# Kernel tuning notes

Measured on AMD Instinct MI355X. Metric: run time of the kernel, lower is better.

## Reference

```python
import jax, jax.numpy as jnp
import numpy as np

# ---- PGA G(3,0,1) tables (metric: e0^2=0, e1^2=e2^2=e3^2=1) ----
METRIC = np.array([0.0, 1.0, 1.0, 1.0])
BLADES = [(), (0,), (1,), (2,), (3,), (0, 1), (0, 2), (0, 3), (1, 2), (1, 3),
          (2, 3), (0, 1, 2), (0, 1, 3), (0, 2, 3), (1, 2, 3), (0, 1, 2, 3)]
IDX = {b: i for i, b in enumerate(BLADES)}


def _sort_sign(lst):
    lst = list(lst)
    sign = 1
    for i in range(len(lst)):
        for j in range(len(lst) - 1 - i):
            if lst[j] > lst[j + 1]:
                lst[j], lst[j + 1] = lst[j + 1], lst[j]
                sign = -sign
    return lst, sign


def _gp(a, b):
    lst, sign = _sort_sign(list(a) + list(b))
    coef = float(sign)
    out, i = [], 0
    while i < len(lst):
        if i + 1 < len(lst) and lst[i] == lst[i + 1]:
            coef *= METRIC[lst[i]]
            i += 2
        else:
            out.append(lst[i])
            i += 1
    return tuple(out), coef


def _outer(a, b):
    if set(a) & set(b):
        return (), 0.0
    lst, sign = _sort_sign(list(a) + list(b))
    return tuple(lst), float(sign)


def _build_tables():
    G = np.zeros((16, 16, 16))
    O = np.zeros((16, 16, 16))
    for i, a in enumerate(BLADES):
        for j, b in enumerate(BLADES):
            bl, c = _gp(a, b)
            if c != 0.0:
                G[IDX[bl], i, j] = c
            bl, c = _outer(a, b)
            if c != 0.0:
                O[IDX[bl], i, j] = c
    # right complement dual: a ^ dual(a) = e0123
    D = np.zeros((16, 16))
    for i, a in enumerate(BLADES):
        comp = tuple(sorted(set(range(4)) - set(a)))
        _, s = _outer(a, comp)
        D[IDX[comp], i] = s
    Dinv = np.linalg.inv(D)
    # join(x, y) = undual(dual(x) ^ dual(y))
    J = np.einsum('km,mpq,pi,qj->kij', Dinv, O, D, D)
    # 9 Pin(3,0,1)-equivariant linear basis maps:
    # 5 grade projections + 4 maps (e0 wedge grade-k part without e0)
    B = np.zeros((9, 16, 16))
    grades = [len(b) for b in BLADES]
    for w in range(5):
        for i, g in enumerate(grades):
            if g == w:
                B[w, i, i] = 1.0
    for w in range(4):
        for i, a in enumerate(BLADES):
            if len(a) == w and 0 not in a:
                bl, c = _outer((0,), a)
                B[5 + w, IDX[bl], i] = c
    return jnp.asarray(G), jnp.asarray(J), jnp.asarray(B)


GP_TBL, JOIN_TBL, EQUI_BASIS = _build_tables()


def equi_linear(x, W):
    # x: [..., c, 16], W: [o, c, 9] -> [..., o, 16]
    M = jnp.einsum('ocw,wab->oacb', W, EQUI_BASIS)  # small: [o,16,c,16]
    return jnp.einsum('oacb,...cb->...oa', M, x)


def setup_inputs() -> dict:
    key = jax.random.key(0)
    k1, k2, k3, k4 = jax.random.split(key, 4)
    B, S, C = 8, 8192, 32
    x = jax.random.normal(k1, (B, S, C, 16), dtype=jnp.float32)
    ref_mv = jax.random.normal(k2, (B, S, 1, 16), dtype=jnp.float32)
    W_bil = jax.random.normal(k3, (2 * 32, C, 9), dtype=jnp.float32) / np.sqrt(9 * C)
    W_out = jax.random.normal(k4, (C, 32, 9), dtype=jnp.float32) / np.sqrt(9 * 32)
    return {"x": x, "ref_mv": ref_mv, "W_bil": W_bil, "W_out": W_out}


def reference(x, ref_mv, W_bil, W_out):
    # project hidden channels -> 2*intermediate = 64 channels
    h = equi_linear(x, W_bil)                      # [B,S,64,16]
    lg, rg, lj, rj = jnp.split(h, 4, axis=-2)      # each [B,S,16,16]
    gp = jnp.einsum('kij,...ci,...cj->...ck', GP_TBL, lg, rg)
    jn = ref_mv[..., 14:15] * jnp.einsum('kij,...ci,...cj->...ck', JOIN_TBL, lj, rj)
    y = jnp.concatenate([gp, jn], axis=-2)         # [B,S,32,16]
    return equi_linear(y, W_out)                   # [B,S,32,16]
```

## Files before the change

### kernel.cpp

```cpp
#include <hip/hip_runtime.h>

typedef float v2f __attribute__((ext_vector_type(2)));

namespace pga {
constexpr int MASKA[16] = {0,1,2,4,8,3,5,9,6,10,12,7,11,13,14,15};
constexpr int IMASK[16] = {0,1,2,5,3,6,8,11,4,7,9,12,10,13,14,15};
constexpr int GR[16]    = {0,1,1,1,1,2,2,2,2,2,2,3,3,3,3,4};

constexpr int osign(int a, int b){
  int c = 0;
  for (int j = 0; j < 4; ++j) if ((b>>j)&1)
    for (int i = j+1; i < 4; ++i) if ((a>>i)&1) ++c;
  return (c&1) ? -1 : 1;
}

struct Tab {
  float gpc[16][16]; int gpk[16][16];
  float jnc[16][16]; int jnk[16][16];
};

constexpr Tab build(){
  Tab t{};
  for (int i = 0; i < 16; ++i) for (int j = 0; j < 16; ++j) {
    const int ma = MASKA[i], mb = MASKA[j];
    if (ma & mb & 1) { t.gpc[i][j] = 0.0f; t.gpk[i][j] = 0; }
    else { t.gpk[i][j] = IMASK[ma^mb]; t.gpc[i][j] = (float)osign(ma, mb); }
    const int ua = 15^ma, ub = 15^mb;
    if (ua & ub) { t.jnc[i][j] = 0.0f; t.jnk[i][j] = 0; }
    else {
      const int sa = osign(ma, ua), sb = osign(mb, ub);
      const int m  = ua | ub;
      const int tt = osign(ua, ub);
      const int r  = 15^m;
      const int sr = osign(r, m);
      t.jnk[i][j] = IMASK[r];
      t.jnc[i][j] = (float)(sa*sb*tt*sr);
    }
  }
  return t;
}
constexpr Tab TAB = build();
constexpr int PS[8] = {0,2,3,4,8,9,10,14};
constexpr int PE[8] = {1,5,6,7,11,12,13,15};
}

__device__ __forceinline__ float sel4(float a, float b, float c, float d, int k){
  float lo = (k & 1) ? b : a;
  float hi = (k & 1) ? d : c;
  return (k & 2) ? hi : lo;
}
__device__ __forceinline__ float xadd1(float v){
  return v + __int_as_float(__builtin_amdgcn_update_dpp(0, __float_as_int(v), 0xB1, 0xF, 0xF, false));
}
__device__ __forceinline__ float xadd2(float v){
  return v + __int_as_float(__builtin_amdgcn_update_dpp(0, __float_as_int(v), 0x4E, 0xF, 0xF, false));
}

#define NP 8
#define XS_PITCH 576
#define HS_BASE  4608
#define HS_PPITCH 1284
#define HS_OPITCH 20

template <int Q0>
__device__ __forceinline__ void equi2_half(const float* __restrict__ yb,
                                           const v2f (&WC)[4][9], v2f (&acc)[8]) {
  #pragma unroll
  for (int q = Q0; q < Q0 + 4; ++q) {
    const int s = pga::PS[q], e = pga::PE[q];
    const int js = s - (Q0/4)*8, je = e - (Q0/4)*8;
    float4 s0 = *(const float4*)(yb + s*36);
    float4 s1 = *(const float4*)(yb + s*36 + 4);
    float4 t0 = *(const float4*)(yb + e*36);
    float4 t1 = *(const float4*)(yb + e*36 + 4);
    v2f ys2[4] = { {s0.x,s0.y},{s0.z,s0.w},{s1.x,s1.y},{s1.z,s1.w} };
    v2f ye2[4] = { {t0.x,t0.y},{t0.z,t0.w},{t1.x,t1.y},{t1.z,t1.w} };
    const int gs = pga::GR[s], ge = pga::GR[e];
    #pragma unroll
    for (int cp = 0; cp < 4; ++cp) {
      acc[js] += WC[cp][gs]    * ys2[cp];
      acc[je] += WC[cp][ge]    * ye2[cp];
      acc[je] += WC[cp][4+ge]  * ys2[cp];
    }
  }
}

__launch_bounds__(256, 2)
__global__ void pga_fused(const float* __restrict__ x, const float* __restrict__ refmv,
                          const float* __restrict__ Wb, const float* __restrict__ Wo,
                          float* __restrict__ out)
{
  __shared__ float lds[14880];
  const int tid = threadIdx.x;
  const long long pos0 = (long long)blockIdx.x * NP;

  const int oA = tid >> 2, cbA = tid & 3;
  v2f WA[4][9];
  {
    const float* wb = Wb + (size_t)(oA*32 + cbA*8)*9;
    #pragma unroll
    for (int cp = 0; cp < 4; ++cp)
      #pragma unroll
      for (int w = 0; w < 9; ++w)
        WA[cp][w] = (v2f){ wb[(2*cp)*9 + w], wb[(2*cp+1)*9 + w] };
  }

  {
    const float4* xg = (const float4*)(x + pos0*512);
    #pragma unroll
    for (int r = 0; r < 4; ++r) {
      int idx = tid + 256*r;
      float4 g = xg[idx];
      int p = idx >> 7, c = (idx >> 2) & 31, aq = idx & 3;
      float* b = &lds[p*XS_PITCH + c];
      b[(aq*4+0)*36] = g.x;
      b[(aq*4+1)*36] = g.y;
      b[(aq*4+2)*36] = g.z;
      b[(aq*4+3)*36] = g.w;
    }
  }
  __syncthreads();

  #pragma unroll 1
  for (int p = 0; p < NP; ++p) {
    const float* xb = &lds[p*XS_PITCH + cbA*8];
    v2f acc[16];
    #pragma unroll
    for (int a = 0; a < 16; ++a) acc[a] = (v2f){0.f, 0.f};
    #pragma unroll
    for (int q = 0; q < 8; ++q) {
      const int s = pga::PS[q], e = pga::PE[q];
      float4 s0 = *(const float4*)(xb + s*36);
      float4 s1 = *(const float4*)(xb + s*36 + 4);
      float4 t0 = *(const float4*)(xb + e*36);
      float4 t1 = *(const float4*)(xb + e*36 + 4);
      v2f xs2[4] = { {s0.x,s0.y},{s0.z,s0.w},{s1.x,s1.y},{s1.z,s1.w} };
      v2f xe2[4] = { {t0.x,t0.y},{t0.z,t0.w},{t1.x,t1.y},{t1.z,t1.w} };
      const int gs = pga::GR[s], ge = pga::GR[e];
      #pragma unroll
      for (int cp = 0; cp < 4; ++cp) {
        acc[s] += WA[cp][gs]   * xs2[cp];
        acc[e] += WA[cp][ge]   * xe2[cp];
        acc[e] += WA[cp][4+ge] * xs2[cp];
      }
    }
    float h[16];
    #pragma unroll
    for (int a = 0; a < 16; ++a) h[a] = xadd2(xadd1(acc[a].x + acc[a].y));
    float4 v;
    v.x = sel4(h[0], h[4], h[8],  h[12], cbA);
    v.y = sel4(h[1], h[5], h[9],  h[13], cbA);
    v.z = sel4(h[2], h[6], h[10], h[14], cbA);
    v.w = sel4(h[3], h[7], h[11], h[15], cbA);
    *(float4*)&lds[HS_BASE + p*HS_PPITCH + oA*HS_OPITCH + cbA*4] = v;
  }
  __syncthreads();

  {
    const int half = tid >> 7, pb = (tid >> 4) & 7, cc = tid & 15;
    const float* r0 = &lds[HS_BASE + pb*HS_PPITCH + (half*32 + cc)*HS_OPITCH];
    const float* r1 = r0 + 16*HS_OPITCH;
    float L[16], R[16];
    #pragma unroll
    for (int k = 0; k < 4; ++k) {
      *(float4*)&L[k*4] = *(const float4*)(r0 + k*4);
      *(float4*)&R[k*4] = *(const float4*)(r1 + k*4);
    }
    float acc[16];
    #pragma unroll
    for (int k = 0; k < 16; ++k) acc[k] = 0.f;
    if (half == 0) {
      #pragma unroll
      for (int i = 0; i < 16; ++i)
        #pragma unroll
        for (int j = 0; j < 16; ++j)
          if (pga::TAB.gpc[i][j] != 0.0f)
            acc[pga::TAB.gpk[i][j]] = fmaf(pga::TAB.gpc[i][j]*L[i], R[j], acc[pga::TAB.gpk[i][j]]);
    } else {
      #pragma unroll
      for (int i = 0; i < 16; ++i)
        #pragma unroll
        for (int j = 0; j < 16; ++j)
          if (pga::TAB.jnc[i][j] != 0.0f)
            acc[pga::TAB.jnk[i][j]] = fmaf(pga::TAB.jnc[i][j]*L[i], R[j], acc[pga::TAB.jnk[i][j]]);
      const float s = refmv[(pos0 + pb)*16 + 14];
      #pragma unroll
      for (int k = 0; k < 16; ++k) acc[k] *= s;
    }
    float* yb = &lds[pb*XS_PITCH + (half*16 + cc)];
    #pragma unroll
    for (int a = 0; a < 16; ++a) yb[a*36] = acc[a];
  }

  const int ahC = tid >> 7, oC = (tid >> 2) & 31, cbC = tid & 3;
  v2f WC[4][9];
  {
    const float* wo = Wo + (size_t)(oC*32 + cbC*8)*9;
    #pragma unroll
    for (int cp = 0; cp < 4; ++cp)
      #pragma unroll
      for (int w = 0; w < 9; ++w)
        WC[cp][w] = (v2f){ wo[(2*cp)*9 + w], wo[(2*cp+1)*9 + w] };
  }
  __syncthreads();

  #pragma unroll 1
  for (int p = 0; p < NP; ++p) {
    const float* yb = &lds[p*XS_PITCH + cbC*8];
    v2f acc[8];
    #pragma unroll
    for (int j = 0; j < 8; ++j) acc[j] = (v2f){0.f, 0.f};
    if (ahC == 0) equi2_half<0>(yb, WC, acc);
    else          equi2_half<4>(yb, WC, acc);
    float f[8];
    #pragma unroll
    for (int j = 0; j < 8; ++j) f[j] = xadd2(xadd1(acc[j].x + acc[j].y));
    float2 st;
    st.x = sel4(f[0], f[2], f[4], f[6], cbC);
    st.y = sel4(f[1], f[3], f[5], f[7], cbC);
    *(float2*)&out[(pos0 + p)*512 + oC*16 + ahC*8 + cbC*2] = st;
  }
}

extern "C" void kernel_launch(void* const* d_in, const int* in_sizes, int n_in,
                              void* d_out, int out_size, void* d_ws, size_t ws_size,
                              hipStream_t stream) {
  const float* x  = (const float*)d_in[0];
  const float* rm = (const float*)d_in[1];
  const float* wb = (const float*)d_in[2];
  const float* wo = (const float*)d_in[3];
  float* out = (float*)d_out;
  const int P = in_sizes[0] / 512;
  const int blocks = P / NP;
  pga_fused<<<blocks, 256, 0, stream>>>(x, rm, wb, wo, out);
}
```

Measured before the change: 399.1 us.

## Retile equivariant linears so each thread computes two output channels over half the blades

```diff
diff --git a/kernel.cpp b/kernel.cpp
--- a/kernel.cpp
+++ b/kernel.cpp
@@ -57,31 +57,36 @@
 }
 
 #define NP 8
-#define XS_PITCH 576
-#define HS_BASE  4608
-#define HS_PPITCH 1284
-#define HS_OPITCH 20
-
-template <int Q0>
-__device__ __forceinline__ void equi2_half(const float* __restrict__ yb,
-                                           const v2f (&WC)[4][9], v2f (&acc)[8]) {
-  #pragma unroll
-  for (int q = Q0; q < Q0 + 4; ++q) {
-    const int s = pga::PS[q], e = pga::PE[q];
-    const int js = s - (Q0/4)*8, je = e - (Q0/4)*8;
-    float4 s0 = *(const float4*)(yb + s*36);
-    float4 s1 = *(const float4*)(yb + s*36 + 4);
-    float4 t0 = *(const float4*)(yb + e*36);
-    float4 t1 = *(const float4*)(yb + e*36 + 4);
-    v2f ys2[4] = { {s0.x,s0.y},{s0.z,s0.w},{s1.x,s1.y},{s1.z,s1.w} };
-    v2f ye2[4] = { {t0.x,t0.y},{t0.z,t0.w},{t1.x,t1.y},{t1.z,t1.w} };
-    const int gs = pga::GR[s], ge = pga::GR[e];
-    #pragma unroll
-    for (int cp = 0; cp < 4; ++cp) {
-      acc[js] += WC[cp][gs]    * ys2[cp];
-      acc[je] += WC[cp][ge]    * ye2[cp];
-      acc[je] += WC[cp][4+ge]  * ys2[cp];
-    }
+#define XS_ROW 36
+#define XS_PP  584
+#define HS_BASE 4672
+#define HS_OP   18
+#define HS_PP   1160
+#define LDS_FLOATS 13952
+
+__device__ __forceinline__ void equi_tile(const float* __restrict__ b,
+    const v2f (&W)[2][4][6], const int (&offS)[4], const int (&offE)[4],
+    v2f (&aS)[2][4], v2f (&aE)[2][4])
+{
+  #pragma unroll
+  for (int qi = 0; qi < 4; ++qi) {
+    const int s5 = (qi == 0) ? 0 : 1;
+    const int e5 = (qi == 0) ? 2 : 3;
+    const int z5 = (qi == 0) ? 4 : 5;
+    float4 s0 = *(const float4*)(b + offS[qi]);
+    float4 s1 = *(const float4*)(b + offS[qi] + 4);
+    float4 t0 = *(const float4*)(b + offE[qi]);
+    float4 t1 = *(const float4*)(b + offE[qi] + 4);
+    v2f xs2[4] = { {s0.x,s0.y},{s0.z,s0.w},{s1.x,s1.y},{s1.z,s1.w} };
+    v2f xe2[4] = { {t0.x,t0.y},{t0.z,t0.w},{t1.x,t1.y},{t1.z,t1.w} };
+    #pragma unroll
+    for (int cp = 0; cp < 4; ++cp)
+      #pragma unroll
+      for (int oo = 0; oo < 2; ++oo) {
+        aS[oo][qi] += W[oo][cp][s5] * xs2[cp];
+        aE[oo][qi] += W[oo][cp][e5] * xe2[cp];
+        aE[oo][qi] += W[oo][cp][z5] * xs2[cp];
+      }
   }
 }
 
@@ -90,19 +95,39 @@
                           const float* __restrict__ Wb, const float* __restrict__ Wo,
                           float* __restrict__ out)
 {
-  __shared__ float lds[14880];
+  __shared__ float lds[LDS_FLOATS];
   const int tid = threadIdx.x;
   const long long pos0 = (long long)blockIdx.x * NP;
 
-  const int oA = tid >> 2, cbA = tid & 3;
-  v2f WA[4][9];
-  {
-    const float* wb = Wb + (size_t)(oA*32 + cbA*8)*9;
+  const int cb  = tid & 3;
+  const int ah  = (tid >> 2) & 1;
+  const int ogA = tid >> 3;
+  const int ogC = (tid >> 3) & 15;
+  const int p2  = tid >> 7;
+
+  const int S0t[4] = {0,2,3,4},  S1t[4] = {14,8,9,10};
+  const int E0t[4] = {1,5,6,7},  E1t[4] = {15,11,12,13};
+  int offS[4], offE[4];
+  #pragma unroll
+  for (int qi = 0; qi < 4; ++qi) {
+    offS[qi] = (ah ? S1t[qi] : S0t[qi]) * XS_ROW;
+    offE[qi] = (ah ? E1t[qi] : E0t[qi]) * XS_ROW;
+  }
+  const int WH0[6] = {0,1,1,2,5,6}, WH1[6] = {3,2,4,3,8,7};
+  int W6[6];
+  #pragma unroll
+  for (int s = 0; s < 6; ++s) W6[s] = ah ? WH1[s] : WH0[s];
+  const int mA = ah ? ((cb == 0) ? 14 : (6 + 2*cb)) : 2*cb;
+
+  v2f WA[2][4][6];
+  #pragma unroll
+  for (int oo = 0; oo < 2; ++oo) {
+    const float* wb = Wb + (size_t)((ogA + oo*32)*32 + cb*8)*9;
     #pragma unroll
     for (int cp = 0; cp < 4; ++cp)
       #pragma unroll
-      for (int w = 0; w < 9; ++w)
-        WA[cp][w] = (v2f){ wb[(2*cp)*9 + w], wb[(2*cp+1)*9 + w] };
+      for (int s = 0; s < 6; ++s)
+        WA[oo][cp][s] = (v2f){ wb[(2*cp)*9 + W6[s]], wb[(2*cp+1)*9 + W6[s]] };
   }
 
   {
@@ -112,59 +137,49 @@
       int idx = tid + 256*r;
       float4 g = xg[idx];
       int p = idx >> 7, c = (idx >> 2) & 31, aq = idx & 3;
-      float* b = &lds[p*XS_PITCH + c];
-      b[(aq*4+0)*36] = g.x;
-      b[(aq*4+1)*36] = g.y;
-      b[(aq*4+2)*36] = g.z;
-      b[(aq*4+3)*36] = g.w;
+      float* b = &lds[p*XS_PP + c];
+      b[(aq*4+0)*XS_ROW] = g.x;
+      b[(aq*4+1)*XS_ROW] = g.y;
+      b[(aq*4+2)*XS_ROW] = g.z;
+      b[(aq*4+3)*XS_ROW] = g.w;
     }
   }
   __syncthreads();
 
   #pragma unroll 1
   for (int p = 0; p < NP; ++p) {
-    const float* xb = &lds[p*XS_PITCH + cbA*8];
-    v2f acc[16];
-    #pragma unroll
-    for (int a = 0; a < 16; ++a) acc[a] = (v2f){0.f, 0.f};
-    #pragma unroll
-    for (int q = 0; q < 8; ++q) {
-      const int s = pga::PS[q], e = pga::PE[q];
-      float4 s0 = *(const float4*)(xb + s*36);
-      float4 s1 = *(const float4*)(xb + s*36 + 4);
-      float4 t0 = *(const float4*)(xb + e*36);
-      float4 t1 = *(const float4*)(xb + e*36 + 4);
-      v2f xs2[4] = { {s0.x,s0.y},{s0.z,s0.w},{s1.x,s1.y},{s1.z,s1.w} };
-      v2f xe2[4] = { {t0.x,t0.y},{t0.z,t0.w},{t1.x,t1.y},{t1.z,t1.w} };
-      const int gs = pga::GR[s], ge = pga::GR[e];
-      #pragma unroll
-      for (int cp = 0; cp < 4; ++cp) {
-        acc[s] += WA[cp][gs]   * xs2[cp];
-        acc[e] += WA[cp][ge]   * xe2[cp];
-        acc[e] += WA[cp][4+ge] * xs2[cp];
+    const float* xb = &lds[p*XS_PP + cb*8];
+    v2f aS[2][4], aE[2][4];
+    #pragma unroll
+    for (int oo = 0; oo < 2; ++oo)
+      #pragma unroll
+      for (int qi = 0; qi < 4; ++qi) { aS[oo][qi] = (v2f){0.f,0.f}; aE[oo][qi] = (v2f){0.f,0.f}; }
+    equi_tile(xb, WA, offS, offE, aS, aE);
+    #pragma unroll
+    for (int oo = 0; oo < 2; ++oo) {
+      float hS[4], hE[4];
+      #pragma unroll
+      for (int qi = 0; qi < 4; ++qi) {
+        hS[qi] = xadd2(xadd1(aS[oo][qi].x + aS[oo][qi].y));
+        hE[qi] = xadd2(xadd1(aE[oo][qi].x + aE[oo][qi].y));
       }
-    }
-    float h[16];
-    #pragma unroll
-    for (int a = 0; a < 16; ++a) h[a] = xadd2(xadd1(acc[a].x + acc[a].y));
-    float4 v;
-    v.x = sel4(h[0], h[4], h[8],  h[12], cbA);
-    v.y = sel4(h[1], h[5], h[9],  h[13], cbA);
-    v.z = sel4(h[2], h[6], h[10], h[14], cbA);
-    v.w = sel4(h[3], h[7], h[11], h[15], cbA);
-    *(float4*)&lds[HS_BASE + p*HS_PPITCH + oA*HS_OPITCH + cbA*4] = v;
+      float2 st = { sel4(hS[0],hS[1],hS[2],hS[3],cb), sel4(hE[0],hE[1],hE[2],hE[3],cb) };
+      *(float2*)&lds[HS_BASE + p*HS_PP + (ogA + oo*32)*HS_OP + mA] = st;
+    }
   }
   __syncthreads();
 
   {
     const int half = tid >> 7, pb = (tid >> 4) & 7, cc = tid & 15;
-    const float* r0 = &lds[HS_BASE + pb*HS_PPITCH + (half*32 + cc)*HS_OPITCH];
-    const float* r1 = r0 + 16*HS_OPITCH;
+    const float* r0 = &lds[HS_BASE + pb*HS_PP + (half*32 + cc)*HS_OP];
+    const float* r1 = r0 + 16*HS_OP;
     float L[16], R[16];
     #pragma unroll
     for (int k = 0; k < 4; ++k) {
-      *(float4*)&L[k*4] = *(const float4*)(r0 + k*4);
-      *(float4*)&R[k*4] = *(const float4*)(r1 + k*4);
+      float4 f = *(const float4*)(r0 + 4*k);
+      L[pga::PS[2*k]] = f.x; L[pga::PE[2*k]] = f.y; L[pga::PS[2*k+1]] = f.z; L[pga::PE[2*k+1]] = f.w;
+      float4 g = *(const float4*)(r1 + 4*k);
+      R[pga::PS[2*k]] = g.x; R[pga::PE[2*k]] = g.y; R[pga::PS[2*k+1]] = g.z; R[pga::PE[2*k+1]] = g.w;
     }
     float acc[16];
     #pragma unroll
@@ -187,38 +202,45 @@
       #pragma unroll
       for (int k = 0; k < 16; ++k) acc[k] *= s;
     }
-    float* yb = &lds[pb*XS_PITCH + (half*16 + cc)];
-    #pragma unroll
-    for (int a = 0; a < 16; ++a) yb[a*36] = acc[a];
-  }
-
-  const int ahC = tid >> 7, oC = (tid >> 2) & 31, cbC = tid & 3;
-  v2f WC[4][9];
-  {
-    const float* wo = Wo + (size_t)(oC*32 + cbC*8)*9;
+    float* yb = &lds[pb*XS_PP + (half*16 + cc)];
+    #pragma unroll
+    for (int a = 0; a < 16; ++a) yb[a*XS_ROW] = acc[a];
+  }
+
+  v2f WC[2][4][6];
+  #pragma unroll
+  for (int oo = 0; oo < 2; ++oo) {
+    const float* wo = Wo + (size_t)((ogC + oo*16)*32 + cb*8)*9;
     #pragma unroll
     for (int cp = 0; cp < 4; ++cp)
       #pragma unroll
-      for (int w = 0; w < 9; ++w)
-        WC[cp][w] = (v2f){ wo[(2*cp)*9 + w], wo[(2*cp+1)*9 + w] };
+      for (int s = 0; s < 6; ++s)
+        WC[oo][cp][s] = (v2f){ wo[(2*cp)*9 + W6[s]], wo[(2*cp+1)*9 + W6[s]] };
   }
   __syncthreads();
 
   #pragma unroll 1
-  for (int p = 0; p < NP; ++p) {
-    const float* yb = &lds[p*XS_PITCH + cbC*8];
-    v2f acc[8];
-    #pragma unroll
-    for (int j = 0; j < 8; ++j) acc[j] = (v2f){0.f, 0.f};
-    if (ahC == 0) equi2_half<0>(yb, WC, acc);
-    else          equi2_half<4>(yb, WC, acc);
-    float f[8];
-    #pragma unroll
-    for (int j = 0; j < 8; ++j) f[j] = xadd2(xadd1(acc[j].x + acc[j].y));
-    float2 st;
-    st.x = sel4(f[0], f[2], f[4], f[6], cbC);
-    st.y = sel4(f[1], f[3], f[5], f[7], cbC);
-    *(float2*)&out[(pos0 + p)*512 + oC*16 + ahC*8 + cbC*2] = st;
+  for (int it = 0; it < 4; ++it) {
+    const int p = it*2 + p2;
+    const float* yb = &lds[p*XS_PP + cb*8];
+    v2f aS[2][4], aE[2][4];
+    #pragma unroll
+    for (int oo = 0; oo < 2; ++oo)
+      #pragma unroll
+      for (int qi = 0; qi < 4; ++qi) { aS[oo][qi] = (v2f){0.f,0.f}; aE[oo][qi] = (v2f){0.f,0.f}; }
+    equi_tile(yb, WC, offS, offE, aS, aE);
+    #pragma unroll
+    for (int oo = 0; oo < 2; ++oo) {
+      float hS[4], hE[4];
+      #pragma unroll
+      for (int qi = 0; qi < 4; ++qi) {
+        hS[qi] = xadd2(xadd1(aS[oo][qi].x + aS[oo][qi].y));
+        hE[qi] = xadd2(xadd1(aE[oo][qi].x + aE[oo][qi].y));
+      }
+      float c0 = ah ? sel4(hS[1],hS[3],hE[2],hS[0],cb) : sel4(hS[0],hS[1],hS[3],hE[2],cb);
+      float c1 = ah ? sel4(hS[2],hE[1],hE[3],hE[0],cb) : sel4(hE[0],hS[2],hE[1],hE[3],cb);
+      *(float2*)&out[(pos0 + p)*512 + (ogC + oo*16)*16 + ah*8 + 2*cb] = (float2){c0, c1};
+    }
   }
 }
 
@@ -229,8 +251,8 @@
   const float* rm = (const float*)d_in[1];
   const float* wb = (const float*)d_in[2];
   const float* wo = (const float*)d_in[3];
-  float* out = (float*)d_out;
+  float* outp = (float*)d_out;
   const int P = in_sizes[0] / 512;
   const int blocks = P / NP;
-  pga_fused<<<blocks, 256, 0, stream>>>(x, rm, wb, wo, out);
-}
+  pga_fused<<<blocks, 256, 0, stream>>>(x, rm, wb, wo, outp);
+}
```

Measured after the change: 537.6 us. 1.35x slower.
